# Kernel optimization log

Hardware: AMD Instinct MI355X
Metric: run time of the kernel (lower is better)

The kernel has to match this reference:

```python
import jax, jax.numpy as jnp
import numpy as np
from jax import lax

STRIDE = (1, 1)
PADDING = ((1, 1), (1, 1))  # stride=1, padding=1 for 3x3 conv


def setup_inputs() -> dict:
    key = jax.random.key(0)
    k1, k2 = jax.random.split(key)
    x = jax.random.normal(k1, (16, 32, 224, 224), dtype=jnp.float32)
    # kaiming_normal_(mode='fan_out', nonlinearity='relu'): std = sqrt(2/fan_out)
    fan_out = 32 * 3 * 3
    weight = jax.random.normal(k2, (32, 32, 3, 3), dtype=jnp.float32) * np.sqrt(2.0 / fan_out)
    return {"x": x, "weight": weight}


def reference(x, weight):
    # absmax 8-bit activation fake-quant
    x_scale = jnp.abs(x).max() + 1e-5
    x_q = jnp.round(jnp.clip(x * 127.0 / x_scale, -128.0, 127.0))
    # BitNet b1.58 ternary weight fake-quant
    w_scale = jnp.abs(weight).mean() + 1e-5
    w_q = jnp.clip(jnp.round(weight / w_scale), -1.0, 1.0)
    # straight-through estimator (no-op in pure forward, kept for fidelity)
    w_ste = weight + lax.stop_gradient(w_q * w_scale - weight)
    x_ste = x + lax.stop_gradient(x_q * (x_scale / 127.0) - x)
    out = lax.conv_general_dilated(
        x_ste, w_ste,
        window_strides=STRIDE,
        padding=PADDING,
        dimension_numbers=("NCHW", "OIHW", "NCHW"),
    )
    return out
```

## Files before the change

kernel.cpp:

```cpp
#include <hip/hip_runtime.h>


typedef __attribute__((ext_vector_type(8))) short short8;
typedef __attribute__((ext_vector_type(4))) float f32x4;

#define HW    224
#define NCH   32
#define PLANE (HW * HW)
#define TH 16
#define TW 32
#define PAIR_F4 802816
#define SLICE_F4 3136

__device__ __forceinline__ int lds_h(int pix, int c) {
    int sw = (pix & 3) ^ ((pix >> 2) & 3);
    return pix * 32 + (c & 7) + ((((c >> 3) ^ sw) & 3) << 3);
}

__device__ __forceinline__ unsigned short q8(float v) {
    float q = rintf(fminf(127.f, fmaxf(-128.f, v)));
    return (unsigned short)(__float_as_uint(q) >> 16);
}


__global__ __launch_bounds__(256) void absmax_kernel(const float* __restrict__ x,
                                                     const float* __restrict__ w,
                                                     unsigned* __restrict__ slots,
                                                     float* __restrict__ scal,
                                                     unsigned short* __restrict__ wbuf)
{
    int tid = threadIdx.x;
    int lane = tid & 63, wv = tid >> 6;

    if (blockIdx.x == 2048) {
        float s = 0.f;
        for (int i = tid; i < 9216; i += 256) s += fabsf(w[i]);
        #pragma unroll
        for (int off = 32; off > 0; off >>= 1) s += __shfl_xor(s, off);
        __shared__ float sm[4];
        __shared__ float s_ws;
        if (lane == 0) sm[wv] = s;
        __syncthreads();
        if (tid == 0) {
            float wscale = (sm[0] + sm[1] + sm[2] + sm[3]) / 9216.f + 1e-5f;
            scal[0] = wscale;
            s_ws = wscale;
        }
        __syncthreads();
        float wscale = s_ws;
        for (int o = tid; o < 9216; o += 256) {
            int frag = o >> 9, rem = o & 511;
            int l = rem >> 3, j = rem & 7;
            int tap = frag >> 1, kb = frag & 1;
            int kout = kb * 16 + (l & 15);
            int c = ((l >> 4) << 3) + j;
            int r = tap / 3, ss = tap % 3;
            float wv2 = w[((kout * 32 + c) * 3 + r) * 3 + ss];
            float q = fminf(1.f, fmaxf(-1.f, rintf(wv2 / wscale)));
            wbuf[o] = (unsigned short)(__float_as_uint(q) >> 16);
        }
        return;
    }

    int p = blockIdx.x & 7;
    int q = blockIdx.x >> 3;
    const float4* x4 = (const float4*)x + (long)p * PAIR_F4 + (255 - q) * SLICE_F4;
    float m = 0.f;
    for (int i = tid; i < SLICE_F4; i += 256) {
        float4 v = x4[i];
        m = fmaxf(m, fmaxf(fmaxf(fabsf(v.x), fabsf(v.y)),
                           fmaxf(fabsf(v.z), fabsf(v.w))));
    }
    #pragma unroll
    for (int off = 32; off > 0; off >>= 1)
        m = fmaxf(m, __shfl_xor(m, off));
    __shared__ float wm[4];
    if (lane == 0) wm[wv] = m;
    __syncthreads();
    if (tid == 0) {
        m = fmaxf(fmaxf(wm[0], wm[1]), fmaxf(wm[2], wm[3]));
        slots[blockIdx.x] = __float_as_uint(m);
    }
}

__global__ __launch_bounds__(512, 2) void conv_kernel(const float* __restrict__ x,
                                                      const unsigned short* __restrict__ wbuf,
                                                      const unsigned* __restrict__ slots,
                                                      const float* __restrict__ scal,
                                                      float* __restrict__ out)
{
    __shared__ __align__(16) unsigned short xs[612 * 32];
    __shared__ float sred[8];

    int bid = (blockIdx.x & 7) * 196 + (blockIdx.x >> 3);
    int tw = bid % 7;
    int rest = bid / 7;
    int th = rest % 14;
    int n  = rest / 14;
    int h0 = th * TH, w0 = tw * TW;

    int tid = threadIdx.x;
    int lane = tid & 63, wv = tid >> 6;

    const float* xn = x + n * (NCH * PLANE);

    int slot = tid & 7;
    int c = (tid >> 3) & 31;
    int hbase = (tid >> 8) * 9;
    const float* tb = xn + c * PLANE + w0 + slot * 4;
    int pixb = 1 + slot * 4;

    uint4 sv = ((const uint4*)slots)[tid];
    float wscale = scal[0];

    float hv[3];
    #pragma unroll
    for (int it = 0; it < 3; ++it) {
        int e = tid + it * 512;
        hv[it] = 0.f;
        if (e < 1152) {
            int side = e & 1, cc = (e >> 1) & 31, hp = e >> 6;
            int gh = h0 - 1 + hp;
            int gw = side ? (w0 + TW) : (w0 - 1);
            int ghc = gh < 0 ? 0 : (gh > HW - 1 ? HW - 1 : gh);
            int gwc = gw < 0 ? 0 : (gw > HW - 1 ? HW - 1 : gw);
            hv[it] = xn[cc * PLANE + ghc * HW + gwc];
        }
    }
    float4 va[5], vb[4];
    #pragma unroll
    for (int i = 0; i < 5; ++i) {
        int gh = h0 - 1 + hbase + i;
        int ghc = gh < 0 ? 0 : (gh > HW - 1 ? HW - 1 : gh);
        va[i] = *(const float4*)(tb + ghc * HW);
    }
    #pragma unroll
    for (int i = 0; i < 4; ++i) {
        int gh = h0 + 4 + hbase + i;
        int ghc = gh < 0 ? 0 : (gh > HW - 1 ? HW - 1 : gh);
        vb[i] = *(const float4*)(tb + ghc * HW);
    }

    float m2 = fmaxf(fmaxf(__uint_as_float(sv.x), __uint_as_float(sv.y)),
                     fmaxf(__uint_as_float(sv.z), __uint_as_float(sv.w)));
    #pragma unroll
    for (int off = 32; off > 0; off >>= 1)
        m2 = fmaxf(m2, __shfl_xor(m2, off));
    if (lane == 0) sred[wv] = m2;
    __syncthreads();
    float xmax = fmaxf(fmaxf(fmaxf(sred[0], sred[1]), fmaxf(sred[2], sred[3])),
                       fmaxf(fmaxf(sred[4], sred[5]), fmaxf(sred[6], sred[7])));
    float xscale = xmax + 1e-5f;
    float inv = 127.f / xscale;
    float osc = (xscale / 127.f) * wscale;

    #pragma unroll
    for (int i = 0; i < 5; ++i) {
        int gh = h0 - 1 + hbase + i;
        float vs = ((unsigned)gh < (unsigned)HW) ? inv : 0.f;
        int p0 = (hbase + i) * 34 + pixb;
        xs[lds_h(p0 + 0, c)] = q8(va[i].x * vs);
        xs[lds_h(p0 + 1, c)] = q8(va[i].y * vs);
        xs[lds_h(p0 + 2, c)] = q8(va[i].z * vs);
        xs[lds_h(p0 + 3, c)] = q8(va[i].w * vs);
    }
    #pragma unroll
    for (int it = 0; it < 3; ++it) {
        int e = tid + it * 512;
        if (e < 1152) {
            int side = e & 1, cc = (e >> 1) & 31, hp = e >> 6;
            int gh = h0 - 1 + hp;
            int gw = side ? (w0 + TW) : (w0 - 1);
            float vs = ((unsigned)gh < (unsigned)HW && (unsigned)gw < (unsigned)HW)
                           ? inv : 0.f;
            xs[lds_h(hp * 34 + (side ? 33 : 0), cc)] = q8(hv[it] * vs);
        }
    }
    #pragma unroll
    for (int i = 0; i < 4; ++i) {
        int gh = h0 + 4 + hbase + i;
        float vs = ((unsigned)gh < (unsigned)HW) ? inv : 0.f;
        int p0 = (hbase + 5 + i) * 34 + pixb;
        xs[lds_h(p0 + 0, c)] = q8(vb[i].x * vs);
        xs[lds_h(p0 + 1, c)] = q8(vb[i].y * vs);
        xs[lds_h(p0 + 2, c)] = q8(vb[i].z * vs);
        xs[lds_h(p0 + 3, c)] = q8(vb[i].w * vs);
    }
    __syncthreads();

    int ln = lane & 15, cb = lane >> 4;
    f32x4 acc[2][2][2] = {};
    const short8* wfp = (const short8*)wbuf;
    short8 wa = wfp[lane];
    short8 wb = wfp[64 + lane];
    for (int tap = 0; tap < 9; ++tap) {
        short8 na, nb;
        if (tap < 8) {
            na = wfp[(2 * tap + 2) * 64 + lane];
            nb = wfp[(2 * tap + 3) * 64 + lane];
        }
        int r = tap / 3;
        int s2 = tap - r * 3;
        #pragma unroll
        for (int ri = 0; ri < 2; ++ri) {
            #pragma unroll
            for (int pb = 0; pb < 2; ++pb) {
                int pix = (wv * 2 + ri + r) * 34 + pb * 16 + ln + s2;
                int sw = (pix & 3) ^ ((pix >> 2) & 3);
                const short8 a = *(const short8*)&xs[pix * 32 + (((cb ^ sw) & 3) << 3)];
                acc[ri][pb][0] = __builtin_amdgcn_mfma_f32_16x16x32_bf16(
                    a, wa, acc[ri][pb][0], 0, 0, 0);
                acc[ri][pb][1] = __builtin_amdgcn_mfma_f32_16x16x32_bf16(
                    a, wb, acc[ri][pb][1], 0, 0, 0);
            }
        }
        wa = na;
        wb = nb;
    }

    float* on = out + n * (NCH * PLANE);
    #pragma unroll
    for (int ri = 0; ri < 2; ++ri) {
        int h = h0 + wv * 2 + ri;
        #pragma unroll
        for (int pb = 0; pb < 2; ++pb) {
            int wcol = w0 + pb * 16 + cb * 4;
            #pragma unroll
            for (int kb = 0; kb < 2; ++kb) {
                int k = kb * 16 + ln;
                f32x4 o;
                o[0] = acc[ri][pb][kb][0] * osc;
                o[1] = acc[ri][pb][kb][1] * osc;
                o[2] = acc[ri][pb][kb][2] * osc;
                o[3] = acc[ri][pb][kb][3] * osc;
                *(f32x4*)&on[(k * HW + h) * HW + wcol] = o;
            }
        }
    }
}

extern "C" void kernel_launch(void* const* d_in, const int* in_sizes, int n_in,
                              void* d_out, int out_size, void* d_ws, size_t ws_size,
                              hipStream_t stream)
{
    const float* x = (const float*)d_in[0];
    const float* w = (const float*)d_in[1];
    float* outp = (float*)d_out;
    unsigned* slots = (unsigned*)d_ws;
    float* scal = (float*)((char*)d_ws + 8192);
    unsigned short* wbuf = (unsigned short*)((char*)d_ws + 8448);

    absmax_kernel<<<2049, 256, 0, stream>>>(x, w, slots, scal, wbuf);
    conv_kernel<<<16 * 14 * 7, 512, 0, stream>>>(x, wbuf, slots, scal, outp);
}
```

Baseline: 84.47 us.

## Fuse absmax and conv into persistent cooperative kernel with grid sync

Replaces the two-kernel absmax-then-conv pipeline with a single cooperative persistent kernel of 512 blocks. Each block reduces a slice of x and part of the weight quantization, then a grid-wide sync is followed by a dynamic atomic tile scheduler per XCD over smaller 8x32 output tiles. This is meant to remove a kernel launch and the tail between the kernels, at the cost of a grid barrier and a smaller tile with more halo overhead. The old two-kernel path is kept as a fallback when cooperative launch fails.

```diff
diff --git a/kernel.cpp b/kernel.cpp
--- a/kernel.cpp
+++ b/kernel.cpp
@@ -1,4 +1,7 @@
 #include <hip/hip_runtime.h>
+#include <hip/hip_cooperative_groups.h>
+
+namespace cg = cooperative_groups;
 
 
 typedef __attribute__((ext_vector_type(8))) short short8;
@@ -7,10 +10,10 @@
 #define HW    224
 #define NCH   32
 #define PLANE (HW * HW)
-#define TH 16
-#define TW 32
+#define TW    32
+#define NX4   (16 * NCH * PLANE / 4)
 #define PAIR_F4 802816
-#define SLICE_F4 3136
+#define SLICE 12544
 
 __device__ __forceinline__ int lds_h(int pix, int c) {
     int sw = (pix & 3) ^ ((pix >> 2) & 3);
@@ -22,12 +25,185 @@
     return (unsigned short)(__float_as_uint(q) >> 16);
 }
 
-
-__global__ __launch_bounds__(256) void absmax_kernel(const float* __restrict__ x,
-                                                     const float* __restrict__ w,
-                                                     unsigned* __restrict__ slots,
-                                                     float* __restrict__ scal,
-                                                     unsigned short* __restrict__ wbuf)
+__global__ __launch_bounds__(512, 2) void fused_kernel(const float* __restrict__ x,
+                                                       const float* __restrict__ w,
+                                                       float* __restrict__ out,
+                                                       unsigned char* __restrict__ wsb)
+{
+    unsigned* slots = (unsigned*)wsb;
+    unsigned* cnt = (unsigned*)(wsb + 2048);
+    unsigned short* wbuf = (unsigned short*)(wsb + 2176);
+
+    __shared__ __align__(16) unsigned short xs[340 * 32];
+    __shared__ float sredA[8], sredB[8];
+    __shared__ int s_tile;
+
+    int tid = threadIdx.x, lane = tid & 63, wv = tid >> 6;
+    int bx = blockIdx.x;
+
+    if (tid == 0 && bx < 8) cnt[bx] = 0u;
+
+    float s = 0.f;
+    #pragma unroll
+    for (int k = 0; k < 18; ++k) s += fabsf(w[tid + 512 * k]);
+
+    const float4* xsl = (const float4*)x + (long)(bx & 7) * PAIR_F4 + (bx >> 3) * SLICE;
+    float m = 0.f;
+    for (int i = tid; i < SLICE; i += 512) {
+        float4 v = xsl[i];
+        m = fmaxf(m, fmaxf(fmaxf(fabsf(v.x), fabsf(v.y)),
+                           fmaxf(fabsf(v.z), fabsf(v.w))));
+    }
+    #pragma unroll
+    for (int off = 32; off; off >>= 1) {
+        s += __shfl_xor(s, off);
+        m = fmaxf(m, __shfl_xor(m, off));
+    }
+    if (lane == 0) { sredA[wv] = m; sredB[wv] = s; }
+    __syncthreads();
+    float bm = fmaxf(fmaxf(fmaxf(sredA[0], sredA[1]), fmaxf(sredA[2], sredA[3])),
+                     fmaxf(fmaxf(sredA[4], sredA[5]), fmaxf(sredA[6], sredA[7])));
+    float wsum = ((sredB[0] + sredB[1]) + (sredB[2] + sredB[3])) +
+                 ((sredB[4] + sredB[5]) + (sredB[6] + sredB[7]));
+    float wscale = wsum / 9216.f + 1e-5f;
+    if (tid == 0) slots[bx] = __float_as_uint(bm);
+    if (tid < 18) {
+        int o = bx * 18 + tid;
+        int frag = o >> 9, rem = o & 511;
+        int l = rem >> 3, j = rem & 7;
+        int tap = frag >> 1, kb = frag & 1;
+        int kout = kb * 16 + (l & 15);
+        int c = ((l >> 4) << 3) + j;
+        int r = tap / 3, ss = tap % 3;
+        float wv2 = w[((kout * 32 + c) * 3 + r) * 3 + ss];
+        float q = fminf(1.f, fmaxf(-1.f, rintf(wv2 / wscale)));
+        wbuf[o] = (unsigned short)(__float_as_uint(q) >> 16);
+    }
+
+    cg::this_grid().sync();
+
+    float m2 = __uint_as_float(slots[tid & 511]);
+    #pragma unroll
+    for (int off = 32; off; off >>= 1) m2 = fmaxf(m2, __shfl_xor(m2, off));
+    if (lane == 0) sredA[wv] = m2;
+    __syncthreads();
+    float xmax = fmaxf(fmaxf(fmaxf(sredA[0], sredA[1]), fmaxf(sredA[2], sredA[3])),
+                       fmaxf(fmaxf(sredA[4], sredA[5]), fmaxf(sredA[6], sredA[7])));
+    float xscale = xmax + 1e-5f;
+    float inv = 127.f / xscale;
+    float osc = (xscale / 127.f) * wscale;
+
+    int xcd = bx & 7;
+    const short8* wfp = (const short8*)wbuf;
+    int slot = tid & 7;
+    int c2 = (tid >> 3) & 31;
+    int half = (tid >> 8) & 1;
+    int pixb = 1 + slot * 4;
+    int ln = lane & 15, cb = lane >> 4;
+
+    for (;;) {
+        __syncthreads();
+        if (tid == 0) s_tile = (int)atomicAdd(&cnt[xcd], 1u);
+        __syncthreads();
+        int t = s_tile;
+        if (t >= 392) break;
+        int n = 2 * xcd + (t >= 196);
+        int tt = (t >= 196) ? t - 196 : t;
+        int th = tt / 7, tw = tt - th * 7;
+        int h0 = th * 8, w0 = tw * TW;
+        const float* xn = x + n * (NCH * PLANE);
+        const float* tb = xn + c2 * PLANE + w0 + slot * 4;
+
+        float4 va[5];
+        float hv[2];
+        #pragma unroll
+        for (int i = 0; i < 5; ++i) {
+            int gh = h0 - 1 + half * 5 + i;
+            int ghc = gh < 0 ? 0 : (gh > HW - 1 ? HW - 1 : gh);
+            va[i] = *(const float4*)(tb + ghc * HW);
+        }
+        #pragma unroll
+        for (int rep = 0; rep < 2; ++rep) {
+            int e = tid + rep * 512;
+            hv[rep] = 0.f;
+            if (e < 640) {
+                int side = e & 1, cc = (e >> 1) & 31, hp = e >> 6;
+                int gh = h0 - 1 + hp;
+                int gw = side ? (w0 + TW) : (w0 - 1);
+                int ghc = gh < 0 ? 0 : (gh > HW - 1 ? HW - 1 : gh);
+                int gwc = gw < 0 ? 0 : (gw > HW - 1 ? HW - 1 : gw);
+                hv[rep] = xn[cc * PLANE + ghc * HW + gwc];
+            }
+        }
+        #pragma unroll
+        for (int i = 0; i < 5; ++i) {
+            int gh = h0 - 1 + half * 5 + i;
+            float vs = ((unsigned)gh < (unsigned)HW) ? inv : 0.f;
+            int p0 = (half * 5 + i) * 34 + pixb;
+            xs[lds_h(p0 + 0, c2)] = q8(va[i].x * vs);
+            xs[lds_h(p0 + 1, c2)] = q8(va[i].y * vs);
+            xs[lds_h(p0 + 2, c2)] = q8(va[i].z * vs);
+            xs[lds_h(p0 + 3, c2)] = q8(va[i].w * vs);
+        }
+        #pragma unroll
+        for (int rep = 0; rep < 2; ++rep) {
+            int e = tid + rep * 512;
+            if (e < 640) {
+                int side = e & 1, cc = (e >> 1) & 31, hp = e >> 6;
+                int gh = h0 - 1 + hp;
+                int gw = side ? (w0 + TW) : (w0 - 1);
+                float vs = ((unsigned)gh < (unsigned)HW && (unsigned)gw < (unsigned)HW)
+                               ? inv : 0.f;
+                xs[lds_h(hp * 34 + (side ? 33 : 0), cc)] = q8(hv[rep] * vs);
+            }
+        }
+        __syncthreads();
+
+        f32x4 acc[2][2] = {};
+        short8 wa = wfp[lane];
+        short8 wb = wfp[64 + lane];
+        for (int tap = 0; tap < 9; ++tap) {
+            short8 na, nb;
+            if (tap < 8) {
+                na = wfp[(2 * tap + 2) * 64 + lane];
+                nb = wfp[(2 * tap + 3) * 64 + lane];
+            }
+            int r = tap / 3, s2 = tap - r * 3;
+            #pragma unroll
+            for (int pb = 0; pb < 2; ++pb) {
+                int pix = (wv + r) * 34 + pb * 16 + ln + s2;
+                int sw = (pix & 3) ^ ((pix >> 2) & 3);
+                const short8 a = *(const short8*)&xs[pix * 32 + (((cb ^ sw) & 3) << 3)];
+                acc[pb][0] = __builtin_amdgcn_mfma_f32_16x16x32_bf16(a, wa, acc[pb][0], 0, 0, 0);
+                acc[pb][1] = __builtin_amdgcn_mfma_f32_16x16x32_bf16(a, wb, acc[pb][1], 0, 0, 0);
+            }
+            wa = na; wb = nb;
+        }
+
+        float* on = out + n * (NCH * PLANE);
+        int h = h0 + wv;
+        #pragma unroll
+        for (int pb = 0; pb < 2; ++pb) {
+            int wcol = w0 + pb * 16 + cb * 4;
+            #pragma unroll
+            for (int kb = 0; kb < 2; ++kb) {
+                int k = kb * 16 + ln;
+                f32x4 o;
+                o[0] = acc[pb][kb][0] * osc;
+                o[1] = acc[pb][kb][1] * osc;
+                o[2] = acc[pb][kb][2] * osc;
+                o[3] = acc[pb][kb][3] * osc;
+                *(f32x4*)&on[(k * HW + h) * HW + wcol] = o;
+            }
+        }
+    }
+}
+
+__global__ __launch_bounds__(256) void fb_absmax(const float* __restrict__ x,
+                                                 const float* __restrict__ w,
+                                                 unsigned* __restrict__ slots,
+                                                 float* __restrict__ scal,
+                                                 unsigned short* __restrict__ wbuf)
 {
     int tid = threadIdx.x;
     int lane = tid & 63, wv = tid >> 6;
@@ -61,12 +237,9 @@
         }
         return;
     }
-
-    int p = blockIdx.x & 7;
-    int q = blockIdx.x >> 3;
-    const float4* x4 = (const float4*)x + (long)p * PAIR_F4 + (255 - q) * SLICE_F4;
+    const float4* x4 = (const float4*)x;
     float m = 0.f;
-    for (int i = tid; i < SLICE_F4; i += 256) {
+    for (int i = blockIdx.x * 256 + tid; i < NX4; i += 2048 * 256) {
         float4 v = x4[i];
         m = fmaxf(m, fmaxf(fmaxf(fabsf(v.x), fabsf(v.y)),
                            fmaxf(fabsf(v.z), fabsf(v.w))));
@@ -83,11 +256,11 @@
     }
 }
 
-__global__ __launch_bounds__(512, 2) void conv_kernel(const float* __restrict__ x,
-                                                      const unsigned short* __restrict__ wbuf,
-                                                      const unsigned* __restrict__ slots,
-                                                      const float* __restrict__ scal,
-                                                      float* __restrict__ out)
+__global__ __launch_bounds__(512, 2) void fb_conv(const float* __restrict__ x,
+                                                  const unsigned short* __restrict__ wbuf,
+                                                  const unsigned* __restrict__ slots,
+                                                  const float* __restrict__ scal,
+                                                  float* __restrict__ out)
 {
     __shared__ __align__(16) unsigned short xs[612 * 32];
     __shared__ float sred[8];
@@ -97,11 +270,10 @@
     int rest = bid / 7;
     int th = rest % 14;
     int n  = rest / 14;
-    int h0 = th * TH, w0 = tw * TW;
+    int h0 = th * 16, w0 = tw * TW;
 
     int tid = threadIdx.x;
     int lane = tid & 63, wv = tid >> 6;
-
     const float* xn = x + n * (NCH * PLANE);
 
     int slot = tid & 7;
@@ -246,10 +418,22 @@
     const float* x = (const float*)d_in[0];
     const float* w = (const float*)d_in[1];
     float* outp = (float*)d_out;
-    unsigned* slots = (unsigned*)d_ws;
-    float* scal = (float*)((char*)d_ws + 8192);
-    unsigned short* wbuf = (unsigned short*)((char*)d_ws + 8448);
-
-    absmax_kernel<<<2049, 256, 0, stream>>>(x, w, slots, scal, wbuf);
-    conv_kernel<<<16 * 14 * 7, 512, 0, stream>>>(x, wbuf, slots, scal, outp);
-}
+    unsigned char* wsb = (unsigned char*)d_ws;
+
+    int nb = 0;
+    hipError_t qe = hipOccupancyMaxActiveBlocksPerMultiprocessor(
+        &nb, (const void*)fused_kernel, 512, 0);
+    if (qe == hipSuccess && nb >= 2) {
+        void* args[] = { (void*)&x, (void*)&w, (void*)&outp, (void*)&wsb };
+        hipError_t le = hipLaunchCooperativeKernel((const void*)fused_kernel,
+                                                   dim3(512), dim3(512), args, 0, stream);
+        if (le == hipSuccess) return;
+    }
+    (void)hipGetLastError();
+
+    unsigned* slots = (unsigned*)wsb;
+    float* scal = (float*)(wsb + 8192);
+    unsigned short* wbuf = (unsigned short*)(wsb + 8448);
+    fb_absmax<<<2049, 256, 0, stream>>>(x, w, slots, scal, wbuf);
+    fb_conv<<<16 * 14 * 7, 512, 0, stream>>>(x, wbuf, slots, scal, outp);
+}
```

After: 83.88 us. About the same (-0.7%).

## Halve conv tile height to 8 rows with 256-thread blocks and grid-stride absmax

Applied to the files above, without the earlier changes.

The conv kernel now uses 8x32 output tiles with 256-thread blocks and launch bounds of 4 blocks per CU, doubling the block count and shrinking the LDS staging buffer so more blocks can be resident. The absmax pass changes from a reversed, pair-strided slice per block to a flat grid-stride loop over the whole input, and the conv kernel reads 512 partial maxima as two uint4 per thread. This gives more parallelism and occupancy but raises halo overhead, since 10 input rows are loaded per 8 output rows instead of 18 per 16. The old reversed slice order probably kept recently read data in cache for the conv kernel, and that reuse may be lost.

```diff
diff --git a/kernel.cpp b/kernel.cpp
--- a/kernel.cpp
+++ b/kernel.cpp
@@ -7,10 +7,9 @@
 #define HW    224
 #define NCH   32
 #define PLANE (HW * HW)
-#define TH 16
+#define TH 8
 #define TW 32
-#define PAIR_F4 802816
-#define SLICE_F4 3136
+#define NX4   (16 * NCH * PLANE / 4)
 
 __device__ __forceinline__ int lds_h(int pix, int c) {
     int sw = (pix & 3) ^ ((pix >> 2) & 3);
@@ -62,11 +61,9 @@
         return;
     }
 
-    int p = blockIdx.x & 7;
-    int q = blockIdx.x >> 3;
-    const float4* x4 = (const float4*)x + (long)p * PAIR_F4 + (255 - q) * SLICE_F4;
+    const float4* x4 = (const float4*)x;
     float m = 0.f;
-    for (int i = tid; i < SLICE_F4; i += 256) {
+    for (int i = blockIdx.x * 256 + tid; i < NX4; i += 2048 * 256) {
         float4 v = x4[i];
         m = fmaxf(m, fmaxf(fmaxf(fabsf(v.x), fabsf(v.y)),
                            fmaxf(fabsf(v.z), fabsf(v.w))));
@@ -83,20 +80,20 @@
     }
 }
 
-__global__ __launch_bounds__(512, 2) void conv_kernel(const float* __restrict__ x,
+__global__ __launch_bounds__(256, 4) void conv_kernel(const float* __restrict__ x,
                                                       const unsigned short* __restrict__ wbuf,
                                                       const unsigned* __restrict__ slots,
                                                       const float* __restrict__ scal,
                                                       float* __restrict__ out)
 {
-    __shared__ __align__(16) unsigned short xs[612 * 32];
-    __shared__ float sred[8];
-
-    int bid = (blockIdx.x & 7) * 196 + (blockIdx.x >> 3);
+    __shared__ __align__(16) unsigned short xs[340 * 32];
+    __shared__ float sred[4];
+
+    int bid = (blockIdx.x & 7) * 392 + (blockIdx.x >> 3);
     int tw = bid % 7;
     int rest = bid / 7;
-    int th = rest % 14;
-    int n  = rest / 14;
+    int th = rest % 28;
+    int n  = rest / 28;
     int h0 = th * TH, w0 = tw * TW;
 
     int tid = threadIdx.x;
@@ -105,20 +102,20 @@
     const float* xn = x + n * (NCH * PLANE);
 
     int slot = tid & 7;
-    int c = (tid >> 3) & 31;
-    int hbase = (tid >> 8) * 9;
+    int c = tid >> 3;
     const float* tb = xn + c * PLANE + w0 + slot * 4;
     int pixb = 1 + slot * 4;
 
-    uint4 sv = ((const uint4*)slots)[tid];
+    uint4 s0 = ((const uint4*)slots)[tid];
+    uint4 s1 = ((const uint4*)slots)[tid + 256];
     float wscale = scal[0];
 
     float hv[3];
     #pragma unroll
     for (int it = 0; it < 3; ++it) {
-        int e = tid + it * 512;
+        int e = tid + it * 256;
         hv[it] = 0.f;
-        if (e < 1152) {
+        if (e < 640) {
             int side = e & 1, cc = (e >> 1) & 31, hp = e >> 6;
             int gh = h0 - 1 + hp;
             int gw = side ? (w0 + TW) : (w0 - 1);
@@ -127,38 +124,39 @@
             hv[it] = xn[cc * PLANE + ghc * HW + gwc];
         }
     }
-    float4 va[5], vb[4];
-    #pragma unroll
-    for (int i = 0; i < 5; ++i) {
-        int gh = h0 - 1 + hbase + i;
+    float4 va[5], vb[5];
+    #pragma unroll
+    for (int i = 0; i < 5; ++i) {
+        int gh = h0 - 1 + i;
         int ghc = gh < 0 ? 0 : (gh > HW - 1 ? HW - 1 : gh);
         va[i] = *(const float4*)(tb + ghc * HW);
     }
     #pragma unroll
-    for (int i = 0; i < 4; ++i) {
-        int gh = h0 + 4 + hbase + i;
-        int ghc = gh < 0 ? 0 : (gh > HW - 1 ? HW - 1 : gh);
+    for (int i = 0; i < 5; ++i) {
+        int gh = h0 + 4 + i;
+        int ghc = gh > HW - 1 ? HW - 1 : gh;
         vb[i] = *(const float4*)(tb + ghc * HW);
     }
 
-    float m2 = fmaxf(fmaxf(__uint_as_float(sv.x), __uint_as_float(sv.y)),
-                     fmaxf(__uint_as_float(sv.z), __uint_as_float(sv.w)));
+    float m2 = fmaxf(fmaxf(fmaxf(__uint_as_float(s0.x), __uint_as_float(s0.y)),
+                           fmaxf(__uint_as_float(s0.z), __uint_as_float(s0.w))),
+                     fmaxf(fmaxf(__uint_as_float(s1.x), __uint_as_float(s1.y)),
+                           fmaxf(__uint_as_float(s1.z), __uint_as_float(s1.w))));
     #pragma unroll
     for (int off = 32; off > 0; off >>= 1)
         m2 = fmaxf(m2, __shfl_xor(m2, off));
     if (lane == 0) sred[wv] = m2;
     __syncthreads();
-    float xmax = fmaxf(fmaxf(fmaxf(sred[0], sred[1]), fmaxf(sred[2], sred[3])),
-                       fmaxf(fmaxf(sred[4], sred[5]), fmaxf(sred[6], sred[7])));
+    float xmax = fmaxf(fmaxf(sred[0], sred[1]), fmaxf(sred[2], sred[3]));
     float xscale = xmax + 1e-5f;
     float inv = 127.f / xscale;
     float osc = (xscale / 127.f) * wscale;
 
     #pragma unroll
     for (int i = 0; i < 5; ++i) {
-        int gh = h0 - 1 + hbase + i;
+        int gh = h0 - 1 + i;
         float vs = ((unsigned)gh < (unsigned)HW) ? inv : 0.f;
-        int p0 = (hbase + i) * 34 + pixb;
+        int p0 = i * 34 + pixb;
         xs[lds_h(p0 + 0, c)] = q8(va[i].x * vs);
         xs[lds_h(p0 + 1, c)] = q8(va[i].y * vs);
         xs[lds_h(p0 + 2, c)] = q8(va[i].z * vs);
@@ -166,8 +164,8 @@
     }
     #pragma unroll
     for (int it = 0; it < 3; ++it) {
-        int e = tid + it * 512;
-        if (e < 1152) {
+        int e = tid + it * 256;
+        if (e < 640) {
             int side = e & 1, cc = (e >> 1) & 31, hp = e >> 6;
             int gh = h0 - 1 + hp;
             int gw = side ? (w0 + TW) : (w0 - 1);
@@ -177,10 +175,10 @@
         }
     }
     #pragma unroll
-    for (int i = 0; i < 4; ++i) {
-        int gh = h0 + 4 + hbase + i;
-        float vs = ((unsigned)gh < (unsigned)HW) ? inv : 0.f;
-        int p0 = (hbase + 5 + i) * 34 + pixb;
+    for (int i = 0; i < 5; ++i) {
+        int gh = h0 + 4 + i;
+        float vs = (gh < HW) ? inv : 0.f;
+        int p0 = (5 + i) * 34 + pixb;
         xs[lds_h(p0 + 0, c)] = q8(vb[i].x * vs);
         xs[lds_h(p0 + 1, c)] = q8(vb[i].y * vs);
         xs[lds_h(p0 + 2, c)] = q8(vb[i].z * vs);
@@ -251,5 +249,5 @@
     unsigned short* wbuf = (unsigned short*)((char*)d_ws + 8448);
 
     absmax_kernel<<<2049, 256, 0, stream>>>(x, w, slots, scal, wbuf);
-    conv_kernel<<<16 * 14 * 7, 512, 0, stream>>>(x, wbuf, slots, scal, outp);
-}
+    conv_kernel<<<16 * 28 * 7, 256, 0, stream>>>(x, wbuf, slots, scal, outp);
+}
```

After: 73.48 us. 1.15x faster.
